# Optimization experiments

Hardware: AMD Instinct MI355X
Metric: run time of the kernel (lower is better)

The kernel has to match this reference:

```python
import jax, jax.numpy as jnp
import numpy as np

N = 50000          # nodes
E = 400000         # directed input edges (one direction; symmetrized in reference)
F = 128            # in_channels == feat_size
GW = 128           # gather_width
OUT = 1            # out_channels
NUM_GRAPHS = 50
PROP_ITER = 4


def _lin(key, fi, fo):
    k1, k2 = jax.random.split(key)
    s = 1.0 / np.sqrt(fi)
    W = jax.random.uniform(k1, (fi, fo), minval=-s, maxval=s, dtype=jnp.float32)
    b = jax.random.uniform(k2, (fo,), minval=-s, maxval=s, dtype=jnp.float32)
    return W, b


def setup_inputs() -> dict:
    key = jax.random.key(0)
    ks = jax.random.split(key, 20)
    x = jax.random.normal(ks[0], (N, F), dtype=jnp.float32)
    src = jax.random.randint(ks[1], (E,), 0, N)
    off = jax.random.randint(ks[2], (E,), 1, N)   # avoid self-edges (self loops added in reference)
    dst = (src + off) % N
    edge_index = jnp.stack([src, dst])
    edge_attr = jax.random.uniform(ks[3], (E,), dtype=jnp.float32) * 6.0
    batch = jnp.arange(N) // (N // NUM_GRAPHS)
    gate_W1, gate_b1 = _lin(ks[4], F, F // 2)
    gate_W2, gate_b2 = _lin(ks[5], F // 2, F // 4)
    gate_W3, gate_b3 = _lin(ks[6], F // 4, 1)
    s = 1.0 / np.sqrt(F)
    gru_Wih = jax.random.uniform(ks[7], (3 * F, F), minval=-s, maxval=s, dtype=jnp.float32)
    gru_Whh = jax.random.uniform(ks[8], (3 * F, F), minval=-s, maxval=s, dtype=jnp.float32)
    gru_bih = jax.random.uniform(ks[9], (3 * F,), minval=-s, maxval=s, dtype=jnp.float32)
    gru_bhh = jax.random.uniform(ks[10], (3 * F,), minval=-s, maxval=s, dtype=jnp.float32)
    ai_W1, ai_b1 = _lin(ks[11], 2 * F, F)
    ai_W2, ai_b2 = _lin(ks[12], F, GW)
    aj_W, aj_b = _lin(ks[13], F, GW)
    h1, h2 = int(GW / 1.5), GW // 2
    out_W1, out_b1 = _lin(ks[14], GW, h1)
    out_W2, out_b2 = _lin(ks[15], h1, h2)
    out_W3, out_b3 = _lin(ks[16], h2, OUT)
    t = jnp.array([3.5], dtype=jnp.float32)
    return dict(x=x, edge_index=edge_index, edge_attr=edge_attr, batch=batch, t=t,
                gate_W1=gate_W1, gate_b1=gate_b1, gate_W2=gate_W2, gate_b2=gate_b2,
                gate_W3=gate_W3, gate_b3=gate_b3,
                gru_Wih=gru_Wih, gru_Whh=gru_Whh, gru_bih=gru_bih, gru_bhh=gru_bhh,
                ai_W1=ai_W1, ai_b1=ai_b1, ai_W2=ai_W2, ai_b2=ai_b2,
                aj_W=aj_W, aj_b=aj_b,
                out_W1=out_W1, out_b1=out_b1, out_W2=out_W2, out_b2=out_b2,
                out_W3=out_W3, out_b3=out_b3)


def _softsign(v):
    return v / (1.0 + jnp.abs(v))


def reference(x, edge_index, edge_attr, batch, t,
              gate_W1, gate_b1, gate_W2, gate_b2, gate_W3, gate_b3,
              gru_Wih, gru_Whh, gru_bih, gru_bhh,
              ai_W1, ai_b1, ai_W2, ai_b2, aj_W, aj_b,
              out_W1, out_b1, out_W2, out_b2, out_W3, out_b3):
    n = x.shape[0]
    loops = jnp.arange(n)
    # to_undirected + add_self_loops(fill=1.0); Graph_Cutoff filters edge_attr <= t.
    src = jnp.concatenate([edge_index[0], edge_index[1], loops])
    dst = jnp.concatenate([edge_index[1], edge_index[0], loops])
    feat = jnp.concatenate([edge_attr, edge_attr, jnp.ones((n,), edge_attr.dtype)])
    mask = feat <= t[0]                       # static-shape edge mask == edge filtering
    fmask = mask.astype(x.dtype)

    h = x
    for _ in range(PROP_ITER):
        # AttentionalAggregation gate over messages x_j = h[src]
        g = _softsign(h @ gate_W1 + gate_b1)
        g = _softsign(g @ gate_W2 + gate_b2)
        g = (g @ gate_W3 + gate_b3)[:, 0]     # [N] per-node gate logit
        logits = g[src]                       # [E_tot]
        mx = jax.ops.segment_max(jnp.where(mask, logits, -jnp.inf), dst, num_segments=n)
        mx = jnp.where(jnp.isfinite(mx), mx, 0.0)
        w = jnp.exp(jnp.where(mask, logits - mx[dst], -30.0)) * fmask
        denom = jax.ops.segment_sum(w, dst, num_segments=n)
        alpha = w / jnp.where(denom > 0, denom, 1.0)[dst]
        m = jax.ops.segment_sum(alpha[:, None] * h[src], dst, num_segments=n)  # [N,F]
        # torch.nn.GRUCell(m, h)
        gi = m @ gru_Wih.T + gru_bih
        gh = h @ gru_Whh.T + gru_bhh
        ir, iz, ig = jnp.split(gi, 3, axis=1)
        hr, hz, hg = jnp.split(gh, 3, axis=1)
        r = jax.nn.sigmoid(ir + hr)
        z = jax.nn.sigmoid(iz + hz)
        cand = jnp.tanh(ig + r * hg)
        h = (1.0 - z) * cand + z * h

    # Message_Attention: softmax(net_i([h, x]), axis=1) * net_j(x)
    ai = _softsign(jnp.concatenate([h, x], axis=1) @ ai_W1 + ai_b1)
    ai = _softsign(ai @ ai_W2 + ai_b2)
    attn = jax.nn.softmax(ai, axis=1)
    aj = _softsign(x @ aj_W + aj_b)
    node_out = attn * aj                      # [N, GW]

    pooled = jax.ops.segment_sum(node_out, batch, num_segments=NUM_GRAPHS)
    o = jax.nn.relu(pooled @ out_W1 + out_b1)
    o = jax.nn.relu(o @ out_W2 + out_b2)
    return o @ out_W3 + out_b3                # [NUM_GRAPHS, OUT]
```

## Files before the change

### kernel.cpp

```cpp
#include <hip/hip_runtime.h>
#include <hip/hip_bf16.h>

#define F 128
#define PROP_ITER 4

typedef unsigned short u16;
typedef unsigned int u32;
typedef __attribute__((ext_vector_type(8))) short bf16x8;
typedef __attribute__((ext_vector_type(4))) float f32x4;

__device__ __forceinline__ float softsign(float v) { return __fdividef(v, 1.0f + fabsf(v)); }
__device__ __forceinline__ float fsig(float v)  { return __fdividef(1.0f, 1.0f + __expf(-v)); }
__device__ __forceinline__ float ftanh(float v) { return 1.0f - __fdividef(2.0f, __expf(2.0f * v) + 1.0f); }
__device__ __forceinline__ u16 f2bf(float f) {
    union { float f; unsigned u; } v; v.f = f;
    unsigned r = v.u + 0x7FFF + ((v.u >> 16) & 1);
    return (u16)(r >> 16);
}
__device__ __forceinline__ float bf2f(u32 lo16) {
    union { unsigned u; float f; } v; v.u = lo16 << 16; return v.f;
}

__global__ __launch_bounds__(256) void count_edges(const int* __restrict__ ei,
                                                   const float* __restrict__ ea,
                                                   const float* __restrict__ t,
                                                   int* __restrict__ deg, int E, int N) {
    int i = blockIdx.x * 256 + threadIdx.x;
    int tot = 2 * E + N;
    if (i >= tot) return;
    int dst; float f;
    if (i < E)            { dst = ei[E + i];   f = ea[i]; }
    else if (i < 2 * E)   { dst = ei[i - E];   f = ea[i - E]; }
    else                  { dst = i - 2 * E;   f = 1.0f; }
    if (f <= t[0]) atomicAdd(&deg[dst], 1);
}

__global__ __launch_bounds__(256) void scan_partial(const int* __restrict__ deg,
                                                    int* __restrict__ bsum, int N) {
    __shared__ int sred[256];
    int tid = threadIdx.x;
    int base = blockIdx.x * 2048 + tid * 8;
    int s = 0;
    #pragma unroll
    for (int i = 0; i < 8; i++) {
        int idx = base + i;
        if (idx < N) s += deg[idx];
    }
    sred[tid] = s;
    __syncthreads();
    for (int off = 128; off; off >>= 1) {
        if (tid < off) sred[tid] += sred[tid + off];
        __syncthreads();
    }
    if (tid == 0) bsum[blockIdx.x] = sred[0];
}

__global__ __launch_bounds__(256) void scan_bsum(int* __restrict__ bsum, int nb) {
    __shared__ int s[256];
    int tid = threadIdx.x;
    int v = (tid < nb) ? bsum[tid] : 0;
    s[tid] = v;
    __syncthreads();
    for (int off = 1; off < 256; off <<= 1) {
        int u = (tid >= off) ? s[tid - off] : 0;
        __syncthreads();
        s[tid] += u;
        __syncthreads();
    }
    if (tid < nb) bsum[tid] = s[tid] - v;
    if (tid == 255) bsum[nb] = s[255];
}

__global__ __launch_bounds__(256) void scan_final(const int* __restrict__ deg,
                                                  const int* __restrict__ bsum,
                                                  int* __restrict__ row_ptr,
                                                  int* __restrict__ cursor,
                                                  int N, int nb) {
    __shared__ int sred[256];
    int tid = threadIdx.x;
    int base = blockIdx.x * 2048 + tid * 8;
    int vals[8];
    int s = 0;
    #pragma unroll
    for (int i = 0; i < 8; i++) {
        int idx = base + i;
        vals[i] = (idx < N) ? deg[idx] : 0;
        s += vals[i];
    }
    sred[tid] = s;
    __syncthreads();
    for (int off = 1; off < 256; off <<= 1) {
        int u = (tid >= off) ? sred[tid - off] : 0;
        __syncthreads();
        sred[tid] += u;
        __syncthreads();
    }
    int run = bsum[blockIdx.x] + sred[tid] - s;
    #pragma unroll
    for (int i = 0; i < 8; i++) {
        int idx = base + i;
        if (idx < N) { row_ptr[idx] = run; cursor[idx] = run; run += vals[i]; }
    }
    if (blockIdx.x == 0 && tid == 0) row_ptr[N] = bsum[nb];
}

__global__ __launch_bounds__(256) void scatter_edges(const int* __restrict__ ei,
                                                     const float* __restrict__ ea,
                                                     const float* __restrict__ t,
                                                     int* __restrict__ cursor,
                                                     int* __restrict__ col, int E, int N) {
    int i = blockIdx.x * 256 + threadIdx.x;
    int tot = 2 * E + N;
    if (i >= tot) return;
    int src, dst; float f;
    if (i < E)            { src = ei[i];      dst = ei[E + i]; f = ea[i]; }
    else if (i < 2 * E)   { src = ei[i];      dst = ei[i - E]; f = ea[i - E]; }
    else                  { src = i - 2 * E;  dst = src;       f = 1.0f; }
    if (f <= t[0]) {
        int p = atomicAdd(&cursor[dst], 1);
        col[p] = src;
    }
}

__global__ __launch_bounds__(256) void conv_x(const float* __restrict__ x,
                                              u16* __restrict__ h16,
                                              u16* __restrict__ x16, int n4) {
    int i = blockIdx.x * 256 + threadIdx.x;
    if (i >= n4) return;
    float4 v = reinterpret_cast<const float4*>(x)[i];
    ushort4 u; u.x = f2bf(v.x); u.y = f2bf(v.y); u.z = f2bf(v.z); u.w = f2bf(v.w);
    reinterpret_cast<ushort4*>(h16)[i] = u;
    reinterpret_cast<ushort4*>(x16)[i] = u;
}

__global__ __launch_bounds__(256) void pack_rm_f32(const float* __restrict__ W,
                                                   u16* __restrict__ pk,
                                                   int total, int nk0) {
    int i = blockIdx.x * 256 + threadIdx.x;
    if (i >= total) return;
    int j = i & 7, l = (i >> 3) & 63;
    int rest = i >> 9;
    int k0 = rest % nk0, fb = rest / nk0;
    int K = nk0 * 32;
    int row = fb * 16 + (l & 15);
    int kk = k0 * 32 + (l >> 4) * 8 + j;
    pk[i] = f2bf(W[(size_t)row * K + kk]);
}

__global__ __launch_bounds__(256) void pack_tr_f32(const float* __restrict__ A,
                                                   u16* __restrict__ pk,
                                                   int total, int nk0, int stride) {
    int i = blockIdx.x * 256 + threadIdx.x;
    if (i >= total) return;
    int j = i & 7, l = (i >> 3) & 63;
    int rest = i >> 9;
    int k0 = rest % nk0, fb = rest / nk0;
    int row = fb * 16 + (l & 15);
    int kk = k0 * 32 + (l >> 4) * 8 + j;
    pk[i] = f2bf(A[(size_t)kk * stride + row]);
}

__device__ __forceinline__ void gate_from_lds(const u16* smh, u16* s1,
                                              const u16* __restrict__ pkgW1,
                                              const float* __restrict__ gb1,
                                              const u16* __restrict__ pkgW2,
                                              const float* __restrict__ gb2,
                                              const float* __restrict__ gW3,
                                              const float* __restrict__ gb3,
                                              float* __restrict__ eg,
                                              int node0, int N, int tid) {
    int wave = tid >> 6, lane = tid & 63, r = lane & 15, g = lane >> 4;
    {
        int j = wave * 16 + r;
        f32x4 acc[4];
        #pragma unroll
        for (int ns = 0; ns < 4; ns++) acc[ns] = (f32x4){0, 0, 0, 0};
        #pragma unroll
        for (int k0 = 0; k0 < 4; k0++) {
            bf16x8 b = *reinterpret_cast<const bf16x8*>(pkgW1 + ((size_t)(wave * 4 + k0) * 64 + lane) * 8);
            int sc = (k0 * 4 + g) ^ (r & 7);
            #pragma unroll
            for (int ns = 0; ns < 4; ns++) {
                bf16x8 a = *reinterpret_cast<const bf16x8*>(smh + ((ns * 16 + r) * 16 + sc) * 8);
                acc[ns] = __builtin_amdgcn_mfma_f32_16x16x32_bf16(a, b, acc[ns], 0, 0, 0);
            }
        }
        float bb = gb1[j];
        #pragma unroll
        for (int ns = 0; ns < 4; ns++)
            #pragma unroll
            for (int q = 0; q < 4; q++) {
                int row = ns * 16 + 4 * g + q;
                s1[(row * 8 + ((j >> 3) ^ (row & 7))) * 8 + (j & 7)] = f2bf(softsign(acc[ns][q] + bb));
            }
    }
    __syncthreads();
    {
        int ns = wave;
        float partial[4] = {0.f, 0.f, 0.f, 0.f};
        #pragma unroll
        for (int fsub = 0; fsub < 2; fsub++) {
            f32x4 acc = {0, 0, 0, 0};
            #pragma unroll
            for (int k0 = 0; k0 < 2; k0++) {
                bf16x8 b = *reinterpret_cast<const bf16x8*>(pkgW2 + ((size_t)(fsub * 2 + k0) * 64 + lane) * 8);
                int sc = (k0 * 4 + g) ^ (r & 7);
                bf16x8 a = *reinterpret_cast<const bf16x8*>(s1 + ((ns * 16 + r) * 8 + sc) * 8);
                acc = __builtin_amdgcn_mfma_f32_16x16x32_bf16(a, b, acc, 0, 0, 0);
            }
            float bb = gb2[fsub * 16 + r];
            float w3 = gW3[fsub * 16 + r];
            #pragma unroll
            for (int q = 0; q < 4; q++) partial[q] += softsign(acc[q] + bb) * w3;
        }
        #pragma unroll
        for (int o = 1; o < 16; o <<= 1)
            #pragma unroll
            for (int q = 0; q < 4; q++) partial[q] += __shfl_xor(partial[q], o);
        if (r == 0) {
            #pragma unroll
            for (int q = 0; q < 4; q++) {
                int node = node0 + ns * 16 + 4 * g + q;
                if (node < N) eg[node] = __expf(partial[q] + gb3[0]);
            }
        }
    }
}

__global__ __launch_bounds__(256) void gate_mfma(const u16* __restrict__ h16,
                                                 const u16* __restrict__ pkgW1,
                                                 const float* __restrict__ gb1,
                                                 const u16* __restrict__ pkgW2,
                                                 const float* __restrict__ gb2,
                                                 const float* __restrict__ gW3,
                                                 const float* __restrict__ gb3,
                                                 float* __restrict__ eg, int N) {
    __shared__ __align__(16) u16 smh[64 * 128];
    __shared__ __align__(16) u16 s1[64 * 64];
    int tid = threadIdx.x;
    int node0 = blockIdx.x * 64;
    #pragma unroll
    for (int rr = 0; rr < 4; rr++) {
        int row = rr * 16 + (tid >> 4);
        int c = tid & 15;
        int gn = node0 + row; if (gn >= N) gn = N - 1;
        bf16x8 vh = *reinterpret_cast<const bf16x8*>(h16 + (size_t)gn * F + c * 8);
        *reinterpret_cast<bf16x8*>(smh + (row * 16 + (c ^ (row & 7))) * 8) = vh;
    }
    __syncthreads();
    gate_from_lds(smh, s1, pkgW1, gb1, pkgW2, gb2, gW3, gb3, eg, node0, N, tid);
}

__global__ __launch_bounds__(64) void aggregate(const u16* __restrict__ h16,
                                                const float* __restrict__ eg,
                                                const int* __restrict__ row_ptr,
                                                const int* __restrict__ col,
                                                u16* __restrict__ m16, int N) {
    int dst = blockIdx.x;
    if (dst >= N) return;
    int lane = threadIdx.x;
    int e0 = row_ptr[dst], e1 = row_ptr[dst + 1];
    int g4 = lane >> 4, r = lane & 15;
    float acc[8];
    #pragma unroll
    for (int i = 0; i < 8; i++) acc[i] = 0.f;
    float denom = 0.f;
    for (int e = e0 + g4; e < e1; e += 4) {
        int s = col[e];
        float w = eg[s];
        denom += w;
        bf16x8 hv = *reinterpret_cast<const bf16x8*>(h16 + (size_t)s * F + r * 8);
        #pragma unroll
        for (int i = 0; i < 8; i++) acc[i] += w * bf2f((u32)(u16)hv[i]);
    }
    #pragma unroll
    for (int o = 16; o <= 32; o <<= 1) {
        denom += __shfl_xor(denom, o);
        #pragma unroll
        for (int i = 0; i < 8; i++) acc[i] += __shfl_xor(acc[i], o);
    }
    if (g4 == 0) {
        float inv = __fdividef(1.0f, denom);
        u32 w0 = (u32)f2bf(acc[0] * inv) | ((u32)f2bf(acc[1] * inv) << 16);
        u32 w1 = (u32)f2bf(acc[2] * inv) | ((u32)f2bf(acc[3] * inv) << 16);
        u32 w2 = (u32)f2bf(acc[4] * inv) | ((u32)f2bf(acc[5] * inv) << 16);
        u32 w3 = (u32)f2bf(acc[6] * inv) | ((u32)f2bf(acc[7] * inv) << 16);
        *reinterpret_cast<uint4*>(m16 + (size_t)dst * F + r * 8) = make_uint4(w0, w1, w2, w3);
    }
}

__global__ __launch_bounds__(512) void gru_fused(const u16* __restrict__ m16,
                                                 const u16* __restrict__ h16,
                                                 const u16* __restrict__ pkWih,
                                                 const u16* __restrict__ pkWhh,
                                                 const float* __restrict__ bih,
                                                 const float* __restrict__ bhh,
                                                 u16* __restrict__ h16o,
                                                 const u16* __restrict__ pkgW1,
                                                 const float* __restrict__ gb1,
                                                 const u16* __restrict__ pkgW2,
                                                 const float* __restrict__ gb2,
                                                 const float* __restrict__ gW3,
                                                 const float* __restrict__ gb3,
                                                 float* __restrict__ eg,
                                                 int do_gate, int N) {
    __shared__ __align__(16) u16 sm[64 * 128];
    __shared__ __align__(16) u16 sh[64 * 128];
    __shared__ __align__(16) u16 shn[64 * 128];
    int tid = threadIdx.x;
    int wave = tid >> 6, lane = tid & 63;
    int r = lane & 15, g = lane >> 4;
    int node0 = blockIdx.x * 64;

    #pragma unroll
    for (int rr = 0; rr < 2; rr++) {
        int row = rr * 32 + (tid >> 4);
        int c = tid & 15;
        int gn = node0 + row; if (gn >= N) gn = N - 1;
        bf16x8 vm = *reinterpret_cast<const bf16x8*>(m16 + (size_t)gn * F + c * 8);
        bf16x8 vh = *reinterpret_cast<const bf16x8*>(h16 + (size_t)gn * F + c * 8);
        int sc = c ^ (row & 7);
        *reinterpret_cast<bf16x8*>(sm + (row * 16 + sc) * 8) = vm;
        *reinterpret_cast<bf16x8*>(sh + (row * 16 + sc) * 8) = vh;
    }
    __syncthreads();

    {
        int fsub = wave;
        f32x4 acc[4][4];
        #pragma unroll
        for (int ns = 0; ns < 4; ns++)
            #pragma unroll
            for (int c = 0; c < 4; c++) acc[ns][c] = (f32x4){0, 0, 0, 0};

        bf16x8 A0, A1, A2, A3, A4, A5, B0, B1, B2, B3, B4, B5;
        auto ld = [&](int k0, bf16x8& q0, bf16x8& q1, bf16x8& q2,
                      bf16x8& q3, bf16x8& q4, bf16x8& q5) {
            q0 = *reinterpret_cast<const bf16x8*>(pkWih + ((size_t)((0  + fsub) * 4 + k0) * 64 + lane) * 8);
            q1 = *reinterpret_cast<const bf16x8*>(pkWih + ((size_t)((8  + fsub) * 4 + k0) * 64 + lane) * 8);
            q2 = *reinterpret_cast<const bf16x8*>(pkWih + ((size_t)((16 + fsub) * 4 + k0) * 64 + lane) * 8);
            q3 = *reinterpret_cast<const bf16x8*>(pkWhh + ((size_t)((0  + fsub) * 4 + k0) * 64 + lane) * 8);
            q4 = *reinterpret_cast<const bf16x8*>(pkWhh + ((size_t)((8  + fsub) * 4 + k0) * 64 + lane) * 8);
            q5 = *reinterpret_cast<const bf16x8*>(pkWhh + ((size_t)((16 + fsub) * 4 + k0) * 64 + lane) * 8);
        };
        auto step = [&](int k0, const bf16x8& q0, const bf16x8& q1, const bf16x8& q2,
                        const bf16x8& q3, const bf16x8& q4, const bf16x8& q5) {
            int sc = (k0 * 4 + g) ^ (r & 7);
            #pragma unroll
            for (int ns = 0; ns < 4; ns++) {
                int rowb = (ns * 16 + r) * 16;
                bf16x8 am = *reinterpret_cast<const bf16x8*>(sm + (rowb + sc) * 8);
                bf16x8 ah = *reinterpret_cast<const bf16x8*>(sh + (rowb + sc) * 8);
                acc[ns][0] = __builtin_amdgcn_mfma_f32_16x16x32_bf16(am, q0, acc[ns][0], 0, 0, 0);
                acc[ns][0] = __builtin_amdgcn_mfma_f32_16x16x32_bf16(ah, q3, acc[ns][0], 0, 0, 0);
                acc[ns][1] = __builtin_amdgcn_mfma_f32_16x16x32_bf16(am, q1, acc[ns][1], 0, 0, 0);
                acc[ns][1] = __builtin_amdgcn_mfma_f32_16x16x32_bf16(ah, q4, acc[ns][1], 0, 0, 0);
                acc[ns][2] = __builtin_amdgcn_mfma_f32_16x16x32_bf16(am, q2, acc[ns][2], 0, 0, 0);
                acc[ns][3] = __builtin_amdgcn_mfma_f32_16x16x32_bf16(ah, q5, acc[ns][3], 0, 0, 0);
            }
        };
        ld(0, A0, A1, A2, A3, A4, A5);
        ld(1, B0, B1, B2, B3, B4, B5);
        step(0, A0, A1, A2, A3, A4, A5);
        ld(2, A0, A1, A2, A3, A4, A5);
        step(1, B0, B1, B2, B3, B4, B5);
        ld(3, B0, B1, B2, B3, B4, B5);
        step(2, A0, A1, A2, A3, A4, A5);
        step(3, B0, B1, B2, B3, B4, B5);

        int fj = fsub * 16 + r;
        int chunk = fj >> 3, e = fj & 7;
        float b_r  = bih[fj] + bhh[fj];
        float b_z  = bih[128 + fj] + bhh[128 + fj];
        float bi_g = bih[256 + fj];
        float bh_g = bhh[256 + fj];
        #pragma unroll
        for (int ns = 0; ns < 4; ns++) {
            #pragma unroll
            for (int q = 0; q < 4; q++) {
                int row = ns * 16 + 4 * g + q;
                float rr2 = fsig(acc[ns][0][q] + b_r);
                float z   = fsig(acc[ns][1][q] + b_z);
                float cand = ftanh(acc[ns][2][q] + bi_g + rr2 * (acc[ns][3][q] + bh_g));
                float hv = bf2f((u32)sh[(row * 16 + (chunk ^ (row & 7))) * 8 + e]);
                float hn = (1.0f - z) * cand + z * hv;
                shn[(row * 16 + (chunk ^ (row & 7))) * 8 + e] = f2bf(hn);
            }
        }
    }
    __syncthreads();

    if (do_gate) {
        if (wave >= 4) {
            int tid2 = tid - 256;
            #pragma unroll
            for (int rr = 0; rr < 4; rr++) {
                int row = rr * 16 + (tid2 >> 4);
                int c = tid2 & 15;
                int gn = node0 + row;
                if (gn < N) {
                    bf16x8 v = *reinterpret_cast<const bf16x8*>(shn + (row * 16 + (c ^ (row & 7))) * 8);
                    *reinterpret_cast<bf16x8*>(h16o + (size_t)gn * F + c * 8) = v;
                }
            }
        } else {
            int j = wave * 16 + r;
            f32x4 acc[4];
            #pragma unroll
            for (int ns = 0; ns < 4; ns++) acc[ns] = (f32x4){0, 0, 0, 0};
            #pragma unroll
            for (int k0 = 0; k0 < 4; k0++) {
                bf16x8 b = *reinterpret_cast<const bf16x8*>(pkgW1 + ((size_t)(wave * 4 + k0) * 64 + lane) * 8);
                int sc = (k0 * 4 + g) ^ (r & 7);
                #pragma unroll
                for (int ns = 0; ns < 4; ns++) {
                    bf16x8 a = *reinterpret_cast<const bf16x8*>(shn + ((ns * 16 + r) * 16 + sc) * 8);
                    acc[ns] = __builtin_amdgcn_mfma_f32_16x16x32_bf16(a, b, acc[ns], 0, 0, 0);
                }
            }
            float bb = gb1[j];
            #pragma unroll
            for (int ns = 0; ns < 4; ns++)
                #pragma unroll
                for (int q = 0; q < 4; q++) {
                    int row = ns * 16 + 4 * g + q;
                    sm[(row * 8 + ((j >> 3) ^ (row & 7))) * 8 + (j & 7)] = f2bf(softsign(acc[ns][q] + bb));
                }
        }
        __syncthreads();
        if (wave < 4) {
            int ns = wave;
            float partial[4] = {0.f, 0.f, 0.f, 0.f};
            #pragma unroll
            for (int fsub = 0; fsub < 2; fsub++) {
                f32x4 acc = {0, 0, 0, 0};
                #pragma unroll
                for (int k0 = 0; k0 < 2; k0++) {
                    bf16x8 b = *reinterpret_cast<const bf16x8*>(pkgW2 + ((size_t)(fsub * 2 + k0) * 64 + lane) * 8);
                    int sc = (k0 * 4 + g) ^ (r & 7);
                    bf16x8 a = *reinterpret_cast<const bf16x8*>(sm + ((ns * 16 + r) * 8 + sc) * 8);
                    acc = __builtin_amdgcn_mfma_f32_16x16x32_bf16(a, b, acc, 0, 0, 0);
                }
                float bb = gb2[fsub * 16 + r];
                float w3 = gW3[fsub * 16 + r];
                #pragma unroll
                for (int q = 0; q < 4; q++) partial[q] += softsign(acc[q] + bb) * w3;
            }
            #pragma unroll
            for (int o = 1; o < 16; o <<= 1)
                #pragma unroll
                for (int q = 0; q < 4; q++) partial[q] += __shfl_xor(partial[q], o);
            if (r == 0) {
                #pragma unroll
                for (int q = 0; q < 4; q++) {
                    int node = node0 + ns * 16 + 4 * g + q;
                    if (node < N) eg[node] = __expf(partial[q] + gb3[0]);
                }
            }
        }
    } else {
        #pragma unroll
        for (int rr = 0; rr < 2; rr++) {
            int row = rr * 32 + (tid >> 4);
            int c = tid & 15;
            int gn = node0 + row;
            if (gn < N) {
                bf16x8 v = *reinterpret_cast<const bf16x8*>(shn + (row * 16 + (c ^ (row & 7))) * 8);
                *reinterpret_cast<bf16x8*>(h16o + (size_t)gn * F + c * 8) = v;
            }
        }
    }
}

__global__ __launch_bounds__(256) void attn_fused(const u16* __restrict__ h16,
                                                  const u16* __restrict__ x16,
                                                  const u16* __restrict__ pkW1,
                                                  const float* __restrict__ b1,
                                                  const u16* __restrict__ pkW2,
                                                  const float* __restrict__ b2,
                                                  const u16* __restrict__ pkWj,
                                                  const float* __restrict__ bj,
                                                  float* __restrict__ pooled,
                                                  int N, int npg, int G) {
    __shared__ __align__(16) u16 smh[64 * 128];
    __shared__ __align__(16) u16 sx[64 * 128];
    __shared__ float s_v[64 * 128];
    __shared__ float s_mx[64], s_sum[64];
    __shared__ float s_pool[2][128];
    int tid = threadIdx.x;
    int wave = tid >> 6, lane = tid & 63, r = lane & 15, g = lane >> 4;
    int node0 = blockIdx.x * 64;

    s_pool[tid >> 7][tid & 127] = 0.f;

    #pragma unroll
    for (int rr = 0; rr < 4; rr++) {
        int row = rr * 16 + (tid >> 4);
        int c = tid & 15;
        int gn = node0 + row; if (gn >= N) gn = N - 1;
        bf16x8 vh = *reinterpret_cast<const bf16x8*>(h16 + (size_t)gn * F + c * 8);
        bf16x8 vx = *reinterpret_cast<const bf16x8*>(x16 + (size_t)gn * F + c * 8);
        int sc = c ^ (row & 7);
        *reinterpret_cast<bf16x8*>(smh + (row * 16 + sc) * 8) = vh;
        *reinterpret_cast<bf16x8*>(sx + (row * 16 + sc) * 8) = vx;
    }
    __syncthreads();

    float v1[2][4][4];
    #pragma unroll
    for (int fs = 0; fs < 2; fs++) {
        int fsub = wave * 2 + fs;
        int j = fsub * 16 + r;
        f32x4 acc[4];
        #pragma unroll
        for (int ns = 0; ns < 4; ns++) acc[ns] = (f32x4){0, 0, 0, 0};
        #pragma unroll
        for (int k0 = 0; k0 < 8; k0++) {
            bf16x8 b = *reinterpret_cast<const bf16x8*>(pkW1 + ((size_t)(fsub * 8 + k0) * 64 + lane) * 8);
            const u16* As = (k0 < 4) ? smh : sx;
            int sc = ((k0 & 3) * 4 + g) ^ (r & 7);
            #pragma unroll
            for (int ns = 0; ns < 4; ns++) {
                bf16x8 a = *reinterpret_cast<const bf16x8*>(As + ((ns * 16 + r) * 16 + sc) * 8);
                acc[ns] = __builtin_amdgcn_mfma_f32_16x16x32_bf16(a, b, acc[ns], 0, 0, 0);
            }
        }
        float bb = b1[j];
        #pragma unroll
        for (int ns = 0; ns < 4; ns++)
            #pragma unroll
            for (int q = 0; q < 4; q++) v1[fs][ns][q] = softsign(acc[ns][q] + bb);
    }
    __syncthreads();

    #pragma unroll
    for (int fs = 0; fs < 2; fs++) {
        int j = (wave * 2 + fs) * 16 + r;
        #pragma unroll
        for (int ns = 0; ns < 4; ns++)
            #pragma unroll
            for (int q = 0; q < 4; q++) {
                int row = ns * 16 + 4 * g + q;
                smh[(row * 16 + ((j >> 3) ^ (row & 7))) * 8 + (j & 7)] = f2bf(v1[fs][ns][q]);
            }
    }
    __syncthreads();

    #pragma unroll
    for (int fs = 0; fs < 2; fs++) {
        int fsub = wave * 2 + fs;
        int j = fsub * 16 + r;
        f32x4 acc[4];
        #pragma unroll
        for (int ns = 0; ns < 4; ns++) acc[ns] = (f32x4){0, 0, 0, 0};
        #pragma unroll
        for (int k0 = 0; k0 < 4; k0++) {
            bf16x8 b = *reinterpret_cast<const bf16x8*>(pkW2 + ((size_t)(fsub * 4 + k0) * 64 + lane) * 8);
            int sc = (k0 * 4 + g) ^ (r & 7);
            #pragma unroll
            for (int ns = 0; ns < 4; ns++) {
                bf16x8 a = *reinterpret_cast<const bf16x8*>(smh + ((ns * 16 + r) * 16 + sc) * 8);
                acc[ns] = __builtin_amdgcn_mfma_f32_16x16x32_bf16(a, b, acc[ns], 0, 0, 0);
            }
        }
        float bb = b2[j];
        #pragma unroll
        for (int ns = 0; ns < 4; ns++)
            #pragma unroll
            for (int q = 0; q < 4; q++) {
                int row = ns * 16 + 4 * g + q;
                s_v[row * 128 + (j ^ ((row & 31) << 2))] = softsign(acc[ns][q] + bb);
            }
    }
    __syncthreads();

    {
        int row = tid >> 2, base = (tid & 3) * 32;
        int swz = (row & 31) << 2;
        float mx = -1e30f;
        #pragma unroll
        for (int i = 0; i < 32; i++) mx = fmaxf(mx, s_v[row * 128 + ((base + i) ^ swz)]);
        mx = fmaxf(mx, __shfl_xor(mx, 1));
        mx = fmaxf(mx, __shfl_xor(mx, 2));
        float sum = 0.f;
        #pragma unroll
        for (int i = 0; i < 32; i++) sum += __expf(s_v[row * 128 + ((base + i) ^ swz)] - mx);
        sum += __shfl_xor(sum, 1);
        sum += __shfl_xor(sum, 2);
        if ((tid & 3) == 0) { s_mx[row] = mx; s_sum[row] = sum; }
    }
    __syncthreads();

    int graph0 = node0 / npg;
    #pragma unroll
    for (int fs = 0; fs < 2; fs++) {
        int fsub = wave * 2 + fs;
        int j = fsub * 16 + r;
        f32x4 acc[4];
        #pragma unroll
        for (int ns = 0; ns < 4; ns++) acc[ns] = (f32x4){0, 0, 0, 0};
        #pragma unroll
        for (int k0 = 0; k0 < 4; k0++) {
            bf16x8 b = *reinterpret_cast<const bf16x8*>(pkWj + ((size_t)(fsub * 4 + k0) * 64 + lane) * 8);
            int sc = (k0 * 4 + g) ^ (r & 7);
            #pragma unroll
            for (int ns = 0; ns < 4; ns++) {
                bf16x8 a = *reinterpret_cast<const bf16x8*>(sx + ((ns * 16 + r) * 16 + sc) * 8);
                acc[ns] = __builtin_amdgcn_mfma_f32_16x16x32_bf16(a, b, acc[ns], 0, 0, 0);
            }
        }
        float bb = bj[j];
        float p0 = 0.f, p1 = 0.f;
        #pragma unroll
        for (int ns = 0; ns < 4; ns++)
            #pragma unroll
            for (int q = 0; q < 4; q++) {
                int row = ns * 16 + 4 * g + q;
                int node = node0 + row;
                if (node < N) {
                    float aj = softsign(acc[ns][q] + bb);
                    float vv = s_v[row * 128 + (j ^ ((row & 31) << 2))];
                    float attn = __fdividef(__expf(vv - s_mx[row]), s_sum[row]);
                    float val = attn * aj;
                    if (node / npg == graph0) p0 += val; else p1 += val;
                }
            }
        if (p0 != 0.f) atomicAdd(&s_pool[0][j], p0);
        if (p1 != 0.f) atomicAdd(&s_pool[1][j], p1);
    }
    __syncthreads();

    {
        int b_ = tid >> 7, colj = tid & 127;
        float v = s_pool[b_][colj];
        int gg = graph0 + b_;
        if (v != 0.f && gg < G) atomicAdd(&pooled[(size_t)gg * F + colj], v);
    }
}

__global__ __launch_bounds__(128) void out_mlp(const float* __restrict__ pooled,
                                               const float* __restrict__ W1, const float* __restrict__ b1,
                                               const float* __restrict__ W2, const float* __restrict__ b2,
                                               const float* __restrict__ W3, const float* __restrict__ b3,
                                               float* __restrict__ out, int H1, int H2) {
    __shared__ float sp[128];
    __shared__ float s1[96];
    __shared__ float s2[64];
    int g = blockIdx.x, j = threadIdx.x;
    sp[j] = pooled[g * F + j];
    __syncthreads();
    if (j < H1) {
        float a = b1[j];
        for (int k = 0; k < 128; k++) a += sp[k] * W1[k * H1 + j];
        s1[j] = fmaxf(a, 0.f);
    }
    __syncthreads();
    if (j < H2) {
        float a = b2[j];
        for (int k = 0; k < H1; k++) a += s1[k] * W2[k * H2 + j];
        s2[j] = fmaxf(a, 0.f);
    }
    __syncthreads();
    if (j == 0) {
        float a = b3[0];
        for (int k = 0; k < H2; k++) a += s2[k] * W3[k];
        out[g] = a;
    }
}

extern "C" void kernel_launch(void* const* d_in, const int* in_sizes, int n_in,
                              void* d_out, int out_size, void* d_ws, size_t ws_size,
                              hipStream_t stream) {
    const float* x    = (const float*)d_in[0];
    const int*   ei   = (const int*)  d_in[1];
    const float* ea   = (const float*)d_in[2];
    const float* t    = (const float*)d_in[4];
    const float* gW1  = (const float*)d_in[5];
    const float* gb1  = (const float*)d_in[6];
    const float* gW2  = (const float*)d_in[7];
    const float* gb2  = (const float*)d_in[8];
    const float* gW3  = (const float*)d_in[9];
    const float* gb3  = (const float*)d_in[10];
    const float* Wih  = (const float*)d_in[11];
    const float* Whh  = (const float*)d_in[12];
    const float* bih  = (const float*)d_in[13];
    const float* bhh  = (const float*)d_in[14];
    const float* aiW1 = (const float*)d_in[15];
    const float* aib1 = (const float*)d_in[16];
    const float* aiW2 = (const float*)d_in[17];
    const float* aib2 = (const float*)d_in[18];
    const float* ajW  = (const float*)d_in[19];
    const float* ajb  = (const float*)d_in[20];
    const float* oW1  = (const float*)d_in[21];
    const float* ob1  = (const float*)d_in[22];
    const float* oW2  = (const float*)d_in[23];
    const float* ob2  = (const float*)d_in[24];
    const float* oW3  = (const float*)d_in[25];
    const float* ob3  = (const float*)d_in[26];
    float* out = (float*)d_out;

    const int N = in_sizes[0] / F;
    const int E = in_sizes[2];
    const int G = out_size;
    const int npg = N / G;
    const int H1 = 85, H2 = 64;
    const int Etot = 2 * E + N;

    char* w = (char*)d_ws;
    auto carve = [&](size_t bytes) {
        void* p = (void*)w;
        w += (bytes + 255) & ~(size_t)255;
        return p;
    };
    int*   deg     = (int*)  carve((size_t)N * 4);
    int*   row_ptr = (int*)  carve((size_t)(N + 1) * 4);
    int*   cursor  = (int*)  carve((size_t)N * 4);
    int*   bsum    = (int*)  carve((size_t)512 * 4);
    int*   col     = (int*)  carve((size_t)Etot * 4);
    float* eg      = (float*)carve((size_t)N * 4);
    u16*   m16     = (u16*)  carve((size_t)N * F * 2);
    u16*   h16A    = (u16*)  carve((size_t)N * F * 2);
    u16*   h16B    = (u16*)  carve((size_t)N * F * 2);
    u16*   x16     = (u16*)  carve((size_t)N * F * 2);
    u16*   pkWih   = (u16*)  carve((size_t)384 * F * 2);
    u16*   pkWhh   = (u16*)  carve((size_t)384 * F * 2);
    u16*   pkW1    = (u16*)  carve((size_t)128 * 256 * 2);
    u16*   pkW2    = (u16*)  carve((size_t)128 * 128 * 2);
    u16*   pkWj    = (u16*)  carve((size_t)128 * 128 * 2);
    u16*   pkgW1   = (u16*)  carve((size_t)64 * 128 * 2);
    u16*   pkgW2   = (u16*)  carve((size_t)32 * 64 * 2);
    float* pooled  = (float*)carve((size_t)G * F * 4);
    (void)ws_size; (void)n_in;

    pack_rm_f32<<<(384 * F + 255) / 256, 256, 0, stream>>>(Wih, pkWih, 384 * F, 4);
    pack_rm_f32<<<(384 * F + 255) / 256, 256, 0, stream>>>(Whh, pkWhh, 384 * F, 4);
    pack_tr_f32<<<(128 * 256 + 255) / 256, 256, 0, stream>>>(aiW1, pkW1, 128 * 256, 8, 128);
    pack_tr_f32<<<(128 * 128 + 255) / 256, 256, 0, stream>>>(aiW2, pkW2, 128 * 128, 4, 128);
    pack_tr_f32<<<(128 * 128 + 255) / 256, 256, 0, stream>>>(ajW, pkWj, 128 * 128, 4, 128);
    pack_tr_f32<<<(64 * 128 + 255) / 256, 256, 0, stream>>>(gW1, pkgW1, 64 * 128, 4, 64);
    pack_tr_f32<<<(32 * 64 + 255) / 256, 256, 0, stream>>>(gW2, pkgW2, 32 * 64, 2, 32);
    int n4 = N * F / 4;
    conv_x<<<(n4 + 255) / 256, 256, 0, stream>>>(x, h16A, x16, n4);

    hipMemsetAsync(deg, 0, (size_t)N * 4, stream);
    int eb = (Etot + 255) / 256;
    count_edges<<<eb, 256, 0, stream>>>(ei, ea, t, deg, E, N);
    int nbs = (N + 2047) / 2048;
    scan_partial<<<nbs, 256, 0, stream>>>(deg, bsum, N);
    scan_bsum<<<1, 256, 0, stream>>>(bsum, nbs);
    scan_final<<<nbs, 256, 0, stream>>>(deg, bsum, row_ptr, cursor, N, nbs);
    scatter_edges<<<eb, 256, 0, stream>>>(ei, ea, t, cursor, col, E, N);

    u16* h16c = h16A;
    u16* h16n = h16B;
    int nb64 = (N + 63) / 64;

    gate_mfma<<<nb64, 256, 0, stream>>>(h16c, pkgW1, gb1, pkgW2, gb2, gW3, gb3, eg, N);

    for (int it = 0; it < PROP_ITER; it++) {
        aggregate<<<N, 64, 0, stream>>>(h16c, eg, row_ptr, col, m16, N);
        gru_fused<<<nb64, 512, 0, stream>>>(m16, h16c, pkWih, pkWhh, bih, bhh, h16n,
                                            pkgW1, gb1, pkgW2, gb2, gW3, gb3, eg,
                                            (it < PROP_ITER - 1) ? 1 : 0, N);
        u16* tmp = h16c; h16c = h16n; h16n = tmp;
    }

    hipMemsetAsync(pooled, 0, (size_t)G * F * 4, stream);
    attn_fused<<<nb64, 256, 0, stream>>>(h16c, x16, pkW1, aib1, pkW2, aib2, pkWj, ajb,
                                         pooled, N, npg, G);
    out_mlp<<<G, 128, 0, stream>>>(pooled, oW1, ob1, oW2, ob2, oW3, ob3, out, H1, H2);
}
```

Baseline: 386.1 us.

## Fuse neighbor aggregation into GRU kernel and merge weight packing launches

Removes the separate aggregate kernel: each GRU block now gathers and softmax-normalizes its 64 destination nodes' neighbor features straight into LDS, which eliminates the m16 intermediate round trip and one launch per iteration. Gate weights are double-buffered (egA/egB) because the GRU kernel now reads the old weights while writing new ones. The seven weight-packing launches are merged into one kernel. The cost is a much narrower gather, 8 threads per node walking edges serially inside a 64-node block, so latency hiding and parallelism across the gather may drop compared with one wave per node.

```diff
diff --git a/kernel.cpp b/kernel.cpp
--- a/kernel.cpp
+++ b/kernel.cpp
@@ -133,31 +133,43 @@
     reinterpret_cast<ushort4*>(x16)[i] = u;
 }
 
-__global__ __launch_bounds__(256) void pack_rm_f32(const float* __restrict__ W,
-                                                   u16* __restrict__ pk,
-                                                   int total, int nk0) {
-    int i = blockIdx.x * 256 + threadIdx.x;
-    if (i >= total) return;
+__device__ __forceinline__ void pk_rm(const float* __restrict__ W, u16* __restrict__ pk,
+                                      int i, int nk0) {
     int j = i & 7, l = (i >> 3) & 63;
     int rest = i >> 9;
     int k0 = rest % nk0, fb = rest / nk0;
     int K = nk0 * 32;
-    int row = fb * 16 + (l & 15);
-    int kk = k0 * 32 + (l >> 4) * 8 + j;
-    pk[i] = f2bf(W[(size_t)row * K + kk]);
-}
-
-__global__ __launch_bounds__(256) void pack_tr_f32(const float* __restrict__ A,
-                                                   u16* __restrict__ pk,
-                                                   int total, int nk0, int stride) {
-    int i = blockIdx.x * 256 + threadIdx.x;
-    if (i >= total) return;
+    pk[i] = f2bf(W[(size_t)(fb * 16 + (l & 15)) * K + k0 * 32 + (l >> 4) * 8 + j]);
+}
+__device__ __forceinline__ void pk_tr(const float* __restrict__ A, u16* __restrict__ pk,
+                                      int i, int nk0, int stride) {
     int j = i & 7, l = (i >> 3) & 63;
     int rest = i >> 9;
     int k0 = rest % nk0, fb = rest / nk0;
     int row = fb * 16 + (l & 15);
     int kk = k0 * 32 + (l >> 4) * 8 + j;
     pk[i] = f2bf(A[(size_t)kk * stride + row]);
+}
+
+__global__ __launch_bounds__(256) void pack_all(const float* __restrict__ Wih,
+                                                const float* __restrict__ Whh,
+                                                const float* __restrict__ aiW1,
+                                                const float* __restrict__ aiW2,
+                                                const float* __restrict__ ajW,
+                                                const float* __restrict__ gW1,
+                                                const float* __restrict__ gW2,
+                                                u16* __restrict__ pkWih, u16* __restrict__ pkWhh,
+                                                u16* __restrict__ pkW1, u16* __restrict__ pkW2,
+                                                u16* __restrict__ pkWj, u16* __restrict__ pkgW1,
+                                                u16* __restrict__ pkgW2) {
+    int i = blockIdx.x * 256 + threadIdx.x;
+    if      (i < 49152)  pk_rm(Wih,  pkWih, i, 4);
+    else if (i < 98304)  pk_rm(Whh,  pkWhh, i - 49152, 4);
+    else if (i < 131072) pk_tr(aiW1, pkW1,  i - 98304, 8, 128);
+    else if (i < 147456) pk_tr(aiW2, pkW2,  i - 131072, 4, 128);
+    else if (i < 163840) pk_tr(ajW,  pkWj,  i - 147456, 4, 128);
+    else if (i < 172032) pk_tr(gW1,  pkgW1, i - 163840, 4, 64);
+    else if (i < 174080) pk_tr(gW2,  pkgW2, i - 172032, 2, 32);
 }
 
 __device__ __forceinline__ void gate_from_lds(const u16* smh, u16* s1,
@@ -251,46 +263,10 @@
     gate_from_lds(smh, s1, pkgW1, gb1, pkgW2, gb2, gW3, gb3, eg, node0, N, tid);
 }
 
-__global__ __launch_bounds__(64) void aggregate(const u16* __restrict__ h16,
-                                                const float* __restrict__ eg,
-                                                const int* __restrict__ row_ptr,
-                                                const int* __restrict__ col,
-                                                u16* __restrict__ m16, int N) {
-    int dst = blockIdx.x;
-    if (dst >= N) return;
-    int lane = threadIdx.x;
-    int e0 = row_ptr[dst], e1 = row_ptr[dst + 1];
-    int g4 = lane >> 4, r = lane & 15;
-    float acc[8];
-    #pragma unroll
-    for (int i = 0; i < 8; i++) acc[i] = 0.f;
-    float denom = 0.f;
-    for (int e = e0 + g4; e < e1; e += 4) {
-        int s = col[e];
-        float w = eg[s];
-        denom += w;
-        bf16x8 hv = *reinterpret_cast<const bf16x8*>(h16 + (size_t)s * F + r * 8);
-        #pragma unroll
-        for (int i = 0; i < 8; i++) acc[i] += w * bf2f((u32)(u16)hv[i]);
-    }
-    #pragma unroll
-    for (int o = 16; o <= 32; o <<= 1) {
-        denom += __shfl_xor(denom, o);
-        #pragma unroll
-        for (int i = 0; i < 8; i++) acc[i] += __shfl_xor(acc[i], o);
-    }
-    if (g4 == 0) {
-        float inv = __fdividef(1.0f, denom);
-        u32 w0 = (u32)f2bf(acc[0] * inv) | ((u32)f2bf(acc[1] * inv) << 16);
-        u32 w1 = (u32)f2bf(acc[2] * inv) | ((u32)f2bf(acc[3] * inv) << 16);
-        u32 w2 = (u32)f2bf(acc[4] * inv) | ((u32)f2bf(acc[5] * inv) << 16);
-        u32 w3 = (u32)f2bf(acc[6] * inv) | ((u32)f2bf(acc[7] * inv) << 16);
-        *reinterpret_cast<uint4*>(m16 + (size_t)dst * F + r * 8) = make_uint4(w0, w1, w2, w3);
-    }
-}
-
-__global__ __launch_bounds__(512) void gru_fused(const u16* __restrict__ m16,
-                                                 const u16* __restrict__ h16,
+__global__ __launch_bounds__(512) void gru_fused(const u16* __restrict__ h16,
+                                                 const int* __restrict__ row_ptr,
+                                                 const int* __restrict__ col,
+                                                 const float* __restrict__ egIn,
                                                  const u16* __restrict__ pkWih,
                                                  const u16* __restrict__ pkWhh,
                                                  const float* __restrict__ bih,
@@ -302,7 +278,7 @@
                                                  const float* __restrict__ gb2,
                                                  const float* __restrict__ gW3,
                                                  const float* __restrict__ gb3,
-                                                 float* __restrict__ eg,
+                                                 float* __restrict__ egOut,
                                                  int do_gate, int N) {
     __shared__ __align__(16) u16 sm[64 * 128];
     __shared__ __align__(16) u16 sh[64 * 128];
@@ -317,11 +293,42 @@
         int row = rr * 32 + (tid >> 4);
         int c = tid & 15;
         int gn = node0 + row; if (gn >= N) gn = N - 1;
-        bf16x8 vm = *reinterpret_cast<const bf16x8*>(m16 + (size_t)gn * F + c * 8);
         bf16x8 vh = *reinterpret_cast<const bf16x8*>(h16 + (size_t)gn * F + c * 8);
-        int sc = c ^ (row & 7);
-        *reinterpret_cast<bf16x8*>(sm + (row * 16 + sc) * 8) = vm;
-        *reinterpret_cast<bf16x8*>(sh + (row * 16 + sc) * 8) = vh;
+        *reinterpret_cast<bf16x8*>(sh + (row * 16 + (c ^ (row & 7))) * 8) = vh;
+    }
+
+    {
+        int grp = tid >> 3, r8 = tid & 7;
+        int dst = node0 + grp;
+        float acc[16];
+        #pragma unroll
+        for (int i = 0; i < 16; i++) acc[i] = 0.f;
+        float denom = 0.f;
+        if (dst < N) {
+            int e0 = row_ptr[dst], e1 = row_ptr[dst + 1];
+            for (int e = e0; e < e1; e++) {
+                int s = col[e];
+                float w = egIn[s];
+                denom += w;
+                const u16* hp = h16 + (size_t)s * F + r8 * 16;
+                bf16x8 h0 = *reinterpret_cast<const bf16x8*>(hp);
+                bf16x8 h1 = *reinterpret_cast<const bf16x8*>(hp + 8);
+                #pragma unroll
+                for (int i = 0; i < 8; i++) acc[i]     += w * bf2f((u32)(u16)h0[i]);
+                #pragma unroll
+                for (int i = 0; i < 8; i++) acc[8 + i] += w * bf2f((u32)(u16)h1[i]);
+            }
+        }
+        float inv = (denom > 0.f) ? __fdividef(1.0f, denom) : 0.f;
+        bf16x8 o0, o1;
+        #pragma unroll
+        for (int i = 0; i < 8; i++) o0[i] = (short)f2bf(acc[i] * inv);
+        #pragma unroll
+        for (int i = 0; i < 8; i++) o1[i] = (short)f2bf(acc[8 + i] * inv);
+        int row = grp;
+        int c0 = 2 * r8, c1 = 2 * r8 + 1;
+        *reinterpret_cast<bf16x8*>(sm + (row * 16 + (c0 ^ (row & 7))) * 8) = o0;
+        *reinterpret_cast<bf16x8*>(sm + (row * 16 + (c1 ^ (row & 7))) * 8) = o1;
     }
     __syncthreads();
 
@@ -454,7 +461,7 @@
                 #pragma unroll
                 for (int q = 0; q < 4; q++) {
                     int node = node0 + ns * 16 + 4 * g + q;
-                    if (node < N) eg[node] = __expf(partial[q] + gb3[0]);
+                    if (node < N) egOut[node] = __expf(partial[q] + gb3[0]);
                 }
             }
         }
@@ -717,8 +724,8 @@
     int*   cursor  = (int*)  carve((size_t)N * 4);
     int*   bsum    = (int*)  carve((size_t)512 * 4);
     int*   col     = (int*)  carve((size_t)Etot * 4);
-    float* eg      = (float*)carve((size_t)N * 4);
-    u16*   m16     = (u16*)  carve((size_t)N * F * 2);
+    float* egA     = (float*)carve((size_t)N * 4);
+    float* egB     = (float*)carve((size_t)N * 4);
     u16*   h16A    = (u16*)  carve((size_t)N * F * 2);
     u16*   h16B    = (u16*)  carve((size_t)N * F * 2);
     u16*   x16     = (u16*)  carve((size_t)N * F * 2);
@@ -732,13 +739,8 @@
     float* pooled  = (float*)carve((size_t)G * F * 4);
     (void)ws_size; (void)n_in;
 
-    pack_rm_f32<<<(384 * F + 255) / 256, 256, 0, stream>>>(Wih, pkWih, 384 * F, 4);
-    pack_rm_f32<<<(384 * F + 255) / 256, 256, 0, stream>>>(Whh, pkWhh, 384 * F, 4);
-    pack_tr_f32<<<(128 * 256 + 255) / 256, 256, 0, stream>>>(aiW1, pkW1, 128 * 256, 8, 128);
-    pack_tr_f32<<<(128 * 128 + 255) / 256, 256, 0, stream>>>(aiW2, pkW2, 128 * 128, 4, 128);
-    pack_tr_f32<<<(128 * 128 + 255) / 256, 256, 0, stream>>>(ajW, pkWj, 128 * 128, 4, 128);
-    pack_tr_f32<<<(64 * 128 + 255) / 256, 256, 0, stream>>>(gW1, pkgW1, 64 * 128, 4, 64);
-    pack_tr_f32<<<(32 * 64 + 255) / 256, 256, 0, stream>>>(gW2, pkgW2, 32 * 64, 2, 32);
+    pack_all<<<(174080 + 255) / 256, 256, 0, stream>>>(Wih, Whh, aiW1, aiW2, ajW, gW1, gW2,
+                                                       pkWih, pkWhh, pkW1, pkW2, pkWj, pkgW1, pkgW2);
     int n4 = N * F / 4;
     conv_x<<<(n4 + 255) / 256, 256, 0, stream>>>(x, h16A, x16, n4);
 
@@ -753,16 +755,19 @@
 
     u16* h16c = h16A;
     u16* h16n = h16B;
+    float* egc = egA;
+    float* egn = egB;
     int nb64 = (N + 63) / 64;
 
-    gate_mfma<<<nb64, 256, 0, stream>>>(h16c, pkgW1, gb1, pkgW2, gb2, gW3, gb3, eg, N);
+    gate_mfma<<<nb64, 256, 0, stream>>>(h16c, pkgW1, gb1, pkgW2, gb2, gW3, gb3, egc, N);
 
     for (int it = 0; it < PROP_ITER; it++) {
-        aggregate<<<N, 64, 0, stream>>>(h16c, eg, row_ptr, col, m16, N);
-        gru_fused<<<nb64, 512, 0, stream>>>(m16, h16c, pkWih, pkWhh, bih, bhh, h16n,
-                                            pkgW1, gb1, pkgW2, gb2, gW3, gb3, eg,
+        gru_fused<<<nb64, 512, 0, stream>>>(h16c, row_ptr, col, egc,
+                                            pkWih, pkWhh, bih, bhh, h16n,
+                                            pkgW1, gb1, pkgW2, gb2, gW3, gb3, egn,
                                             (it < PROP_ITER - 1) ? 1 : 0, N);
         u16* tmp = h16c; h16c = h16n; h16n = tmp;
+        float* tg = egc; egc = egn; egn = tg;
     }
 
     hipMemsetAsync(pooled, 0, (size_t)G * F * 4, stream);
```

Measured after the change: 455.9 us. +18.1%, slower.
